# Performance work log

Hardware: AMD Instinct MI355X
Metric: run time of the kernel (lower is better)

## Reference

```python
import jax, jax.numpy as jnp
import numpy as np

PI = 3.141592653589793


def _conv2d(x, w, b=None, pad=0, groups=1):
    out = jax.lax.conv_general_dilated(
        x, w, (1, 1), ((pad, pad), (pad, pad)),
        dimension_numbers=('NCHW', 'OIHW', 'NCHW'), feature_group_count=groups)
    if b is not None:
        out = out + b[None, :, None, None]
    return out


def _l2norm(x, eps=1e-12):
    # torch F.normalize(p=2, dim=1)
    n = jnp.sqrt(jnp.sum(x * x, axis=1, keepdims=True))
    return x / jnp.maximum(n, eps)


def dense_sift(x):
    # Kornia DenseSIFTDescriptor defaults: 8 angular bins, 4x4 spatial bins,
    # spatial_bin_size=4, stride=1, padding=1, rootsift=True, clipval=0.2.
    eps = 1e-10
    nbins = 8
    # SpatialGradient('diff', normalized=False) with replicate padding:
    px = jnp.pad(x, ((0, 0), (0, 0), (0, 0), (1, 1)), mode='edge')
    gx = px[..., 2:] - px[..., :-2]
    py = jnp.pad(x, ((0, 0), (0, 0), (1, 1), (0, 0)), mode='edge')
    gy = py[:, :, 2:, :] - py[:, :, :-2, :]
    mag = jnp.sqrt(gx * gx + gy * gy + eps)
    ori = jnp.arctan2(gy, gx + eps) + 2.0 * PI
    o_big = nbins * ori / (2.0 * PI)
    bo0f = jnp.floor(o_big)
    wo1 = o_big - bo0f
    bo0 = jnp.mod(bo0f, nbins)
    bo1 = jnp.mod(bo0 + 1.0, nbins)
    w0 = (1.0 - wo1) * mag
    w1 = wo1 * mag
    bins = jnp.arange(nbins, dtype=x.dtype).reshape(1, nbins, 1, 1)
    # soft-assign gradient magnitude into 8 orientation bins  (B,8,H,W)
    ang = (bo0 == bins) * w0 + (bo1 == bins) * w1
    # AvgPool2d(4, stride=1, pad=2, count_include_pad=True) -> (B,8,H+1,W+1)
    avg_k = jnp.ones((nbins, 1, 4, 4), x.dtype) / 16.0
    pooled = _conv2d(ang, avg_k, pad=2, groups=nbins)
    # PoolingConv: identity-reshape 4x4 kernel, pad=1 -> 16 shifted copies of 8 chans
    B, _, Hp, Wp = pooled.shape
    H, W = Hp - 1, Wp - 1
    pp = jnp.pad(pooled, ((0, 0), (0, 0), (1, 1), (1, 1)))
    shifts = jnp.stack(
        [pp[:, :, i:i + H, j:j + W] for i in range(4) for j in range(4)], axis=2)
    out = shifts.reshape(B, nbins * 16, H, W)  # channel n = d*16 + i*4 + j
    out = jnp.clip(_l2norm(out), 0.0, 0.2)
    out = _l2norm(out)
    # rootsift: sqrt(L1-normalize + eps)
    l1 = jnp.sum(jnp.abs(out), axis=1, keepdims=True)
    return jnp.sqrt(out / jnp.maximum(l1, 1e-12) + eps)


def joint_bilateral_blur(x, guidance, ksize=5, sigma_color=0.1, sigma_space=1.5):
    # Kornia joint_bilateral_blur, border='reflect', color_distance='l1'
    r = ksize // 2
    ax = jnp.arange(ksize, dtype=x.dtype) - r
    g1 = jnp.exp(-(ax * ax) / (2.0 * sigma_space ** 2))
    g1 = g1 / jnp.sum(g1)
    space_k = jnp.outer(g1, g1)
    H, W = x.shape[-2], x.shape[-1]
    px = jnp.pad(x, ((0, 0), (0, 0), (r, r), (r, r)), mode='reflect')
    pg = jnp.pad(guidance, ((0, 0), (0, 0), (r, r), (r, r)), mode='reflect')
    num = jnp.zeros_like(x)
    den = jnp.zeros((x.shape[0], 1, H, W), x.dtype)
    inv = -0.5 / (sigma_color ** 2)
    for dy in range(ksize):
        for dx in range(ksize):
            gw = pg[:, :, dy:dy + H, dx:dx + W]
            cd = jnp.square(jnp.sum(jnp.abs(gw - guidance), axis=1, keepdims=True))
            k = space_k[dy, dx] * jnp.exp(inv * cd)
            num = num + px[:, :, dy:dy + H, dx:dx + W] * k
            den = den + k
    return num / den


def setup_inputs() -> dict:
    key = jax.random.key(0)
    ks = jax.random.split(key, 7)
    B, H, W = 4, 270, 512
    x = jax.random.uniform(ks[0], (B, 1, H, W), dtype=jnp.float32)
    def winit(k, shape):
        fan_in = shape[1] * shape[2] * shape[3]
        return jax.random.normal(k, shape, dtype=jnp.float32) / np.sqrt(fan_in)
    return {
        'x': x,
        'conv1_w': winit(ks[1], (32, 128, 5, 5)),
        'conv1_b': jax.random.normal(ks[2], (32,), dtype=jnp.float32) * 0.01,
        'conv2_w': winit(ks[3], (8, 32, 3, 3)),
        'conv2_b': jax.random.normal(ks[4], (8,), dtype=jnp.float32) * 0.01,
        'conv3_w': winit(ks[5], (2, 8, 5, 5)),
        'conv3_b': jax.random.normal(ks[6], (2,), dtype=jnp.float32) * 0.01,
    }


def reference(x, conv1_w, conv1_b, conv2_w, conv2_b, conv3_w, conv3_b):
    orig = x
    f = dense_sift(x)
    f = jax.nn.relu(_conv2d(f, conv1_w, conv1_b, pad=2))
    f = jax.nn.relu(_conv2d(f, conv2_w, conv2_b, pad=1))
    f = _conv2d(f, conv3_w, conv3_b, pad=2)
    f = joint_bilateral_blur(f, jnp.concatenate([orig, orig], axis=1))
    u = f[:, 0]
    u = jnp.clip((u - u.min()) / (u.max() - u.min() + 1e-6), 0.0, 1.0)
    u = u * (0.436 * 2.0) - 0.436
    v = f[:, 1]
    v = jnp.clip((v - v.min()) / (v.max() - v.min() + 1e-6), 0.0, 1.0)
    v = v * (0.615 * 2.0) - 0.615
    y = orig[:, 0]
    r = y + 1.14 * v
    g = y - 0.396 * u - 0.581 * v
    b = y + 2.029 * u
    return jnp.stack([r, g, b], axis=1)
```

## Files before the change

kernel.cpp:

```cpp
#include <hip/hip_runtime.h>
#include <hip/hip_bf16.h>

typedef __hip_bfloat16 bf16;
typedef __attribute__((ext_vector_type(8))) short short8v;
typedef __attribute__((ext_vector_type(4))) float f32x4;
typedef __attribute__((ext_vector_type(16))) float f32x16;

#define HH 270
#define WW 512
#define BB 4
#define HP 271
#define WP 513
#define NPIX (HH*WW)
#define NPOOL (HP*WP)
#define TWO_PI 6.28318530717958647692f
#define PLANE ((size_t)BB*NPIX*16)

__global__ void k_wprep(const float* __restrict__ w1, const float* __restrict__ w2,
                        const float* __restrict__ w3, short* __restrict__ apack,
                        short* __restrict__ a2pack, short* __restrict__ a3pack,
                        float* __restrict__ zp) {
    int stride = gridDim.x * blockDim.x;
    int t0 = blockIdx.x * blockDim.x + threadIdx.x;
    for (int i = t0; i < 1024; i += stride) zp[i] = 0.f;
    for (int i = t0; i < 8*25*64*8; i += stride) {
        int idx = i;
        int j    = idx & 7;  idx >>= 3;
        int lane = idx & 63; idx >>= 6;
        int t    = idx % 25;
        int ck   = idx / 25;
        int o = lane & 31;
        int c = ck*16 + (lane >> 5)*8 + j;
        float v = w1[o*3200 + c*25 + t];
        bf16 h = __float2bfloat16(v);
        apack[i] = *reinterpret_cast<short*>(&h);
    }
    for (int i = t0; i < 9*64*8; i += stride) {
        int j = i & 7; int l = (i >> 3) & 63; int tap = i >> 9;
        int o = l & 15; int cin = (l >> 4)*8 + j;
        float v = (o < 8) ? w2[o*288 + cin*9 + tap] : 0.f;
        bf16 h = __float2bfloat16(v);
        a2pack[i] = *reinterpret_cast<short*>(&h);
    }
    for (int i = t0; i < 7*64*8; i += stride) {
        int j = i & 7; int l = (i >> 3) & 63; int grp = i >> 9;
        int o = l & 15; int tap = grp*4 + (l >> 4);
        float v = (o < 2 && tap < 25) ? w3[o*200 + j*25 + tap] : 0.f;
        bf16 h = __float2bfloat16(v);
        a3pack[i] = *reinterpret_cast<short*>(&h);
    }
}

__global__ __launch_bounds__(256) void k_pool(const float* __restrict__ x,
                                              float* __restrict__ pooled) {
    __shared__ float hist[8][19][20];
    const int tx = threadIdx.x & 15, ty = threadIdx.x >> 4;
    const int j0 = blockIdx.x * 16, i0 = blockIdx.y * 16, b = blockIdx.z;
    const float* xb = x + (size_t)b * NPIX;

    for (int i = threadIdx.x; i < 8*19*20; i += 256) ((float*)hist)[i] = 0.f;
    __syncthreads();

    for (int i = threadIdx.x; i < 361; i += 256) {
        int lh = i / 19, lw = i - lh*19;
        int hh = i0 + lh - 2, ww = j0 + lw - 2;
        if (hh >= 0 && hh < HH && ww >= 0 && ww < WW) {
            float gx = xb[hh*WW + (ww+1 < WW ? ww+1 : WW-1)] - xb[hh*WW + (ww-1 >= 0 ? ww-1 : 0)];
            float gy = xb[(hh+1 < HH ? hh+1 : HH-1)*WW + ww] - xb[(hh-1 >= 0 ? hh-1 : 0)*WW + ww];
            float mag  = sqrtf(gx*gx + gy*gy + 1e-10f);
            float ori  = atan2f(gy, gx + 1e-10f) + TWO_PI;
            float obig = ori * (8.0f / TWO_PI);
            float b0f  = floorf(obig);
            float wo1  = obig - b0f;
            int ib0 = ((int)b0f) & 7;
            int ib1 = (ib0 + 1) & 7;
            hist[ib0][lh][lw] += (1.0f - wo1) * mag;
            hist[ib1][lh][lw] += wo1 * mag;
        }
    }
    __syncthreads();

    int i = i0 + ty, j = j0 + tx;
    if (i < HP && j < WP) {
        float a[8];
        #pragma unroll
        for (int c = 0; c < 8; ++c) a[c] = 0.f;
        #pragma unroll
        for (int di = 0; di < 4; ++di)
            #pragma unroll
            for (int dj = 0; dj < 4; ++dj) {
                #pragma unroll
                for (int c = 0; c < 8; ++c)
                    a[c] += hist[c][ty+di][tx+dj];
            }
        float* pb = pooled + (size_t)b*8*NPOOL + i*WP + j;
        const float s = 1.0f/16.0f;
        #pragma unroll
        for (int c = 0; c < 8; ++c) pb[c*NPOOL] = a[c]*s;
    }
}

__global__ __launch_bounds__(256) void k_feat(const float* __restrict__ pooled,
                                              short* __restrict__ f2) {
    __shared__ float T[8][19][19];
    const int tx = threadIdx.x & 15, ty = threadIdx.x >> 4;
    const int w0 = blockIdx.x * 16, h0 = blockIdx.y * 16, b = blockIdx.z;
    const float* pb = pooled + (size_t)b*8*NPOOL;

    for (int i = threadIdx.x; i < 8*361; i += 256) {
        int c = i / 361; int r = i - c*361; int lh = r / 19, lw = r - lh*19;
        int ph = h0 + lh - 1, pw = w0 + lw - 1;
        float v = 0.f;
        if (ph >= 0 && ph < HP && pw >= 0 && pw < WP)
            v = pb[c*NPOOL + ph*WP + pw];
        T[c][lh][lw] = v;
    }
    __syncthreads();

    float s2 = 0.f;
    #pragma unroll
    for (int c = 0; c < 8; ++c)
        #pragma unroll
        for (int i = 0; i < 4; ++i)
            #pragma unroll
            for (int j = 0; j < 4; ++j) {
                float u = T[c][ty+i][tx+j];
                s2 += u*u;
            }
    float inv1 = 1.0f / fmaxf(sqrtf(s2), 1e-12f);

    float sv2 = 0.f, sv1 = 0.f;
    #pragma unroll
    for (int c = 0; c < 8; ++c)
        #pragma unroll
        for (int i = 0; i < 4; ++i)
            #pragma unroll
            for (int j = 0; j < 4; ++j) {
                float u = T[c][ty+i][tx+j];
                float v = fminf(u*inv1, 0.2f);
                sv2 += v*v; sv1 += v;
            }
    float inv2  = 1.0f / fmaxf(sqrtf(sv2), 1e-12f);
    float invl1 = 1.0f / fmaxf(sv1 * inv2, 1e-12f);

    int outv[64];
    #pragma unroll
    for (int c = 0; c < 8; ++c)
        #pragma unroll
        for (int i = 0; i < 4; ++i)
            #pragma unroll
            for (int jj = 0; jj < 2; ++jj) {
                float u0 = T[c][ty+i][tx+jj*2];
                float u1 = T[c][ty+i][tx+jj*2+1];
                float v0 = fminf(u0*inv1, 0.2f) * inv2;
                float v1 = fminf(u1*inv1, 0.2f) * inv2;
                float fo0 = sqrtf(v0*invl1 + 1e-10f);
                float fo1 = sqrtf(v1*invl1 + 1e-10f);
                bf16 hb0 = __float2bfloat16(fo0);
                bf16 hb1 = __float2bfloat16(fo1);
                unsigned lo = *reinterpret_cast<unsigned short*>(&hb0);
                unsigned hi = *reinterpret_cast<unsigned short*>(&hb1);
                outv[c*8 + i*2 + jj] = (int)(lo | (hi << 16));
            }

    int h = h0 + ty, w = w0 + tx;
    if (h < HH) {
        const size_t pix = (size_t)b*NPIX + h*WW + w;
        #pragma unroll
        for (int ck = 0; ck < 8; ++ck) {
            int4* fb = reinterpret_cast<int4*>(f2 + (size_t)ck*PLANE + pix*16);
            int4 v0, v1;
            v0.x = outv[ck*8+0]; v0.y = outv[ck*8+1]; v0.z = outv[ck*8+2]; v0.w = outv[ck*8+3];
            v1.x = outv[ck*8+4]; v1.y = outv[ck*8+5]; v1.z = outv[ck*8+6]; v1.w = outv[ck*8+7];
            fb[0] = v0; fb[1] = v1;
        }
    }
}

__global__ __launch_bounds__(256, 2) void k_conv1(const short* __restrict__ f2,
        const short* __restrict__ apack, const float* __restrict__ bias,
        short* __restrict__ c1o, const short* __restrict__ zp16) {
    __shared__ short S[4][2][4608];
    const int tid = threadIdx.x;
    const int l   = tid & 63;
    const int wid = tid >> 6;
    const int n      = blockIdx.x;
    const int xcd    = n & 7;
    const int t_     = n >> 3;
    const int within = t_ & 7;
    const int g      = (t_ >> 3)*8 + xcd;
    const int b      = g / 34;
    const int ypair  = g - b*34;
    const int h0     = (ypair*2 + (within >> 2)) * 4;
    const int w0     = (within & 3) * 128;
    const int c32 = l & 31;
    const int ksel = l >> 5;
    const int gw0 = w0 + wid*32 - 2;

    short* Sw0 = &S[wid][0][0];
    short* Sw1 = &S[wid][1][0];

    f32x16 acc0 = {0.f};
    f32x16 acc1 = {0.f};
    f32x16 acc2 = {0.f};
    f32x16 acc3 = {0.f};

    auto STAGE = [&](int ck, short* dstbase) {
        const short* plane = f2 + (size_t)ck*PLANE;
        #pragma unroll
        for (int j = 0; j < 9; ++j) {
            int s  = j*64 + l;
            int pr = s / 72;
            int rem = s - pr*72;
            int px = rem >> 1;
            int half = rem & 1;
            int gh = h0 + pr - 2;
            int gw = gw0 + px;
            const short* src = ((unsigned)gh < (unsigned)HH && (unsigned)gw < (unsigned)WW)
                ? plane + (((size_t)b*HH + gh)*WW + gw)*16 + half*8
                : zp16;
            __builtin_amdgcn_global_load_lds(
                (const __attribute__((address_space(1))) void*)src,
                (__attribute__((address_space(3))) void*)(dstbase + j*512), 16, 0, 0);
        }
    };

    STAGE(0, Sw0);

    for (int ck = 0; ck < 8; ++ck) {
        short* cur = (ck & 1) ? Sw1 : Sw0;
        short* nxt = (ck & 1) ? Sw0 : Sw1;
        if (ck < 7) STAGE(ck + 1, nxt);
        asm volatile("s_waitcnt vmcnt(9)" ::: "memory");

        #pragma unroll
        for (int kx = 0; kx < 5; ++kx) {
            const int px = c32 + kx;
            const short* bp = cur + (size_t)px*16 + (size_t)ksel*8;
            short8v Bf[8];
            #pragma unroll
            for (int pr = 0; pr < 8; ++pr)
                Bf[pr] = *reinterpret_cast<const short8v*>(bp + pr*576);
            short8v Af[5];
            #pragma unroll
            for (int ky = 0; ky < 5; ++ky)
                Af[ky] = *reinterpret_cast<const short8v*>(
                    apack + ((size_t)(ck*25 + ky*5 + kx)*64 + l)*8);
            #pragma unroll
            for (int ky = 0; ky < 5; ++ky) {
                acc0 = __builtin_amdgcn_mfma_f32_32x32x16_bf16(Af[ky], Bf[ky+0], acc0, 0, 0, 0);
                acc1 = __builtin_amdgcn_mfma_f32_32x32x16_bf16(Af[ky], Bf[ky+1], acc1, 0, 0, 0);
                acc2 = __builtin_amdgcn_mfma_f32_32x32x16_bf16(Af[ky], Bf[ky+2], acc2, 0, 0, 0);
                acc3 = __builtin_amdgcn_mfma_f32_32x32x16_bf16(Af[ky], Bf[ky+3], acc3, 0, 0, 0);
            }
        }
        asm volatile("s_waitcnt lgkmcnt(0)" ::: "memory");
    }

    const int px = w0 + wid*32 + c32;
    #pragma unroll
    for (int r = 0; r < 4; ++r) {
        int h = h0 + r;
        if (h < HH) {
            const f32x16& A = (r==0) ? acc0 : (r==1) ? acc1 : (r==2) ? acc2 : acc3;
            const size_t rowbase = ((size_t)b*HH + h)*4;
            #pragma unroll
            for (int q = 0; q < 4; ++q) {
                short4 pk;
                short* pkp = (short*)&pk;
                #pragma unroll
                for (int j = 0; j < 4; ++j) {
                    float v = fmaxf(A[q*4 + j] + bias[q*8 + 4*ksel + j], 0.f);
                    bf16 hb = __float2bfloat16(v);
                    pkp[j] = *reinterpret_cast<short*>(&hb);
                }
                *reinterpret_cast<short4*>(c1o + ((rowbase + q)*WW + px)*8 + ksel*4) = pk;
            }
        }
    }
}

__global__ __launch_bounds__(256) void k_conv2m(const short* __restrict__ c1o,
        const short* __restrict__ a2pack, const float* __restrict__ bias,
        short* __restrict__ c2o, const short* __restrict__ zp16) {
    const int tid = threadIdx.x;
    const int l   = tid & 63;
    const int wid = tid >> 6;
    const int h   = blockIdx.y;
    const int b   = blockIdx.z;
    const int w0  = blockIdx.x*256 + wid*64;
    const int col = l & 15;
    const int kg  = l >> 4;

    f32x4 acc0 = {0.f,0.f,0.f,0.f};
    f32x4 acc1 = {0.f,0.f,0.f,0.f};
    f32x4 acc2 = {0.f,0.f,0.f,0.f};
    f32x4 acc3 = {0.f,0.f,0.f,0.f};

    #pragma unroll
    for (int ky = 0; ky < 3; ++ky) {
        int gh = h + ky - 1;
        bool rv = ((unsigned)gh < (unsigned)HH);
        const short* rowb = c1o + (((size_t)b*HH + (rv ? gh : 0))*4 + kg)*WW*8;
        #pragma unroll
        for (int kx = 0; kx < 3; ++kx) {
            short8v A = *reinterpret_cast<const short8v*>(
                a2pack + ((size_t)(ky*3 + kx)*64 + l)*8);
            #pragma unroll
            for (int nt = 0; nt < 4; ++nt) {
                int gw = w0 + nt*16 + col + kx - 1;
                const short* src = (rv && (unsigned)gw < (unsigned)WW)
                    ? rowb + (size_t)gw*8 : zp16;
                short8v B = *reinterpret_cast<const short8v*>(src);
                if (nt == 0) acc0 = __builtin_amdgcn_mfma_f32_16x16x32_bf16(A, B, acc0, 0, 0, 0);
                if (nt == 1) acc1 = __builtin_amdgcn_mfma_f32_16x16x32_bf16(A, B, acc1, 0, 0, 0);
                if (nt == 2) acc2 = __builtin_amdgcn_mfma_f32_16x16x32_bf16(A, B, acc2, 0, 0, 0);
                if (nt == 3) acc3 = __builtin_amdgcn_mfma_f32_16x16x32_bf16(A, B, acc3, 0, 0, 0);
            }
        }
    }

    if (kg < 2) {
        #pragma unroll
        for (int nt = 0; nt < 4; ++nt) {
            const f32x4& A = (nt==0) ? acc0 : (nt==1) ? acc1 : (nt==2) ? acc2 : acc3;
            int px = w0 + nt*16 + col;
            short4 pk;
            short* pkp = (short*)&pk;
            #pragma unroll
            for (int r = 0; r < 4; ++r) {
                float v = fmaxf(A[r] + bias[kg*4 + r], 0.f);
                bf16 hb = __float2bfloat16(v);
                pkp[r] = *reinterpret_cast<short*>(&hb);
            }
            *reinterpret_cast<short4*>(c2o + (((size_t)b*HH + h)*WW + px)*8 + kg*4) = pk;
        }
    }
}

__global__ __launch_bounds__(256) void k_conv3m(const short* __restrict__ c2o,
        const short* __restrict__ a3pack, const float* __restrict__ bias,
        float* __restrict__ c3o, const short* __restrict__ zp16) {
    const int tid = threadIdx.x;
    const int l   = tid & 63;
    const int wid = tid >> 6;
    const int h   = blockIdx.y;
    const int b   = blockIdx.z;
    const int w0  = blockIdx.x*256 + wid*64;
    const int col = l & 15;
    const int kg  = l >> 4;

    f32x4 acc0 = {0.f,0.f,0.f,0.f};
    f32x4 acc1 = {0.f,0.f,0.f,0.f};
    f32x4 acc2 = {0.f,0.f,0.f,0.f};
    f32x4 acc3 = {0.f,0.f,0.f,0.f};

    #pragma unroll
    for (int grp = 0; grp < 7; ++grp) {
        int tap = grp*4 + kg;
        int ky = tap / 5, kx = tap - ky*5;
        int gh = h + ky - 2;
        bool tv = (tap < 25) && ((unsigned)gh < (unsigned)HH);
        const short* rowb = c2o + ((size_t)b*HH + (tv ? gh : 0))*WW*8;
        short8v A = *reinterpret_cast<const short8v*>(
            a3pack + ((size_t)grp*64 + l)*8);
        #pragma unroll
        for (int nt = 0; nt < 4; ++nt) {
            int gw = w0 + nt*16 + col + kx - 2;
            const short* src = (tv && (unsigned)gw < (unsigned)WW)
                ? rowb + (size_t)gw*8 : zp16;
            short8v B = *reinterpret_cast<const short8v*>(src);
            if (nt == 0) acc0 = __builtin_amdgcn_mfma_f32_16x16x32_bf16(A, B, acc0, 0, 0, 0);
            if (nt == 1) acc1 = __builtin_amdgcn_mfma_f32_16x16x32_bf16(A, B, acc1, 0, 0, 0);
            if (nt == 2) acc2 = __builtin_amdgcn_mfma_f32_16x16x32_bf16(A, B, acc2, 0, 0, 0);
            if (nt == 3) acc3 = __builtin_amdgcn_mfma_f32_16x16x32_bf16(A, B, acc3, 0, 0, 0);
        }
    }

    if (kg == 0) {
        #pragma unroll
        for (int nt = 0; nt < 4; ++nt) {
            const f32x4& A = (nt==0) ? acc0 : (nt==1) ? acc1 : (nt==2) ? acc2 : acc3;
            int px = w0 + nt*16 + col;
            c3o[((size_t)b*2 + 0)*NPIX + h*WW + px] = A[0] + bias[0];
            c3o[((size_t)b*2 + 1)*NPIX + h*WW + px] = A[1] + bias[1];
        }
    }
}

__device__ __forceinline__ int refl(int i, int n) {
    if (i < 0) i = -i;
    if (i >= n) i = 2*n - 2 - i;
    return i;
}

__global__ void k_bilat(const float* __restrict__ c3, const float* __restrict__ x,
                        float* __restrict__ outb) {
    int idx = blockIdx.x * blockDim.x + threadIdx.x;
    if (idx >= BB*NPIX) return;
    int b = idx / NPIX;
    int p = idx - b*NPIX;
    int h = p / WW, w = p - h*WW;
    const float* xb = x + (size_t)b*NPIX;
    const float* f0 = c3 + (size_t)b*2*NPIX;
    const float* f1 = f0 + NPIX;

    float e1 = expf(-1.0f/4.5f), e2 = expf(-4.0f/4.5f);
    float sden = 1.0f + 2.f*e1 + 2.f*e2;
    float g1v[5] = { e2/sden, e1/sden, 1.0f/sden, e1/sden, e2/sden };

    float g = xb[p];
    float num0 = 0.f, num1 = 0.f, den = 0.f;
    #pragma unroll
    for (int dy = 0; dy < 5; ++dy) {
        int hh = refl(h + dy - 2, HH);
        #pragma unroll
        for (int dx = 0; dx < 5; ++dx) {
            int wc = refl(w + dx - 2, WW);
            float gs = xb[hh*WW + wc];
            float d = gs - g;
            float k = g1v[dy] * g1v[dx] * expf(-200.0f * d * d);
            num0 += f0[hh*WW + wc] * k;
            num1 += f1[hh*WW + wc] * k;
            den  += k;
        }
    }
    float invd = 1.0f / den;
    outb[(size_t)b*2*NPIX + p]        = num0 * invd;
    outb[(size_t)b*2*NPIX + NPIX + p] = num1 * invd;
}

__global__ void k_minmax1(const float* __restrict__ blur, float4* __restrict__ partial) {
    float umin = 3.0e38f, umax = -3.0e38f, vmin = 3.0e38f, vmax = -3.0e38f;
    for (int i = blockIdx.x*blockDim.x + threadIdx.x; i < BB*NPIX; i += gridDim.x*blockDim.x) {
        int b = i / NPIX; int p = i - b*NPIX;
        float u = blur[(size_t)b*2*NPIX + p];
        float v = blur[(size_t)b*2*NPIX + NPIX + p];
        umin = fminf(umin, u); umax = fmaxf(umax, u);
        vmin = fminf(vmin, v); vmax = fmaxf(vmax, v);
    }
    #pragma unroll
    for (int off = 32; off > 0; off >>= 1) {
        umin = fminf(umin, __shfl_down(umin, off));
        umax = fmaxf(umax, __shfl_down(umax, off));
        vmin = fminf(vmin, __shfl_down(vmin, off));
        vmax = fmaxf(vmax, __shfl_down(vmax, off));
    }
    __shared__ float4 sm[4];
    int lane = threadIdx.x & 63, wid = threadIdx.x >> 6;
    if (lane == 0) sm[wid] = make_float4(umin, umax, vmin, vmax);
    __syncthreads();
    if (threadIdx.x == 0) {
        float4 r = sm[0];
        for (int k = 1; k < 4; ++k) {
            r.x = fminf(r.x, sm[k].x); r.y = fmaxf(r.y, sm[k].y);
            r.z = fminf(r.z, sm[k].z); r.w = fmaxf(r.w, sm[k].w);
        }
        partial[blockIdx.x] = r;
    }
}

__global__ void k_minmax2(const float4* __restrict__ partial, float* __restrict__ sc) {
    float4 p = partial[threadIdx.x];
    #pragma unroll
    for (int off = 32; off > 0; off >>= 1) {
        p.x = fminf(p.x, __shfl_down(p.x, off));
        p.y = fmaxf(p.y, __shfl_down(p.y, off));
        p.z = fminf(p.z, __shfl_down(p.z, off));
        p.w = fmaxf(p.w, __shfl_down(p.w, off));
    }
    __shared__ float4 sm[2];
    if ((threadIdx.x & 63) == 0) sm[threadIdx.x >> 6] = p;
    __syncthreads();
    if (threadIdx.x == 0) {
        sc[0] = fminf(sm[0].x, sm[1].x);
        sc[1] = fmaxf(sm[0].y, sm[1].y);
        sc[2] = fminf(sm[0].z, sm[1].z);
        sc[3] = fmaxf(sm[0].w, sm[1].w);
    }
}

__global__ void k_final(const float* __restrict__ blur, const float* __restrict__ x,
                        const float* __restrict__ sc, float* __restrict__ out) {
    int idx = blockIdx.x * blockDim.x + threadIdx.x;
    if (idx >= BB*NPIX) return;
    int b = idx / NPIX;
    int p = idx - b*NPIX;
    float umin = sc[0], umax = sc[1], vmin = sc[2], vmax = sc[3];
    float u = blur[(size_t)b*2*NPIX + p];
    float v = blur[(size_t)b*2*NPIX + NPIX + p];
    u = fminf(fmaxf((u - umin) / (umax - umin + 1e-6f), 0.f), 1.f) * 0.872f - 0.436f;
    v = fminf(fmaxf((v - vmin) / (vmax - vmin + 1e-6f), 0.f), 1.f) * 1.23f  - 0.615f;
    float y = x[(size_t)b*NPIX + p];
    out[(size_t)(b*3+0)*NPIX + p] = y + 1.14f*v;
    out[(size_t)(b*3+1)*NPIX + p] = y - 0.396f*u - 0.581f*v;
    out[(size_t)(b*3+2)*NPIX + p] = y + 2.029f*u;
}

extern "C" void kernel_launch(void* const* d_in, const int* in_sizes, int n_in,
                              void* d_out, int out_size, void* d_ws, size_t ws_size,
                              hipStream_t stream) {
    const float* x  = (const float*)d_in[0];
    const float* w1 = (const float*)d_in[1];
    const float* b1 = (const float*)d_in[2];
    const float* w2 = (const float*)d_in[3];
    const float* b2 = (const float*)d_in[4];
    const float* w3 = (const float*)d_in[5];
    const float* b3 = (const float*)d_in[6];
    float* out = (float*)d_out;
    char* ws = (char*)d_ws;

    const size_t POOLED_OFF = 0;
    const size_t X_OFF      = 17795072;
    const size_t Y_OFF      = X_OFF + 141557760;
    const size_t AP_OFF     = Y_OFF + 35389440;
    const size_t A2_OFF     = AP_OFF + 204800;
    const size_t A3_OFF     = A2_OFF + 9216;
    const size_t PART_OFF   = A3_OFF + 7168;
    const size_t SC_OFF     = PART_OFF + 2048;
    const size_t ZP_OFF     = SC_OFF + 256;

    float*  pooled = (float*)(ws + POOLED_OFF);
    short*  f2     = (short*)(ws + X_OFF);
    short*  c2o    = (short*)(ws + X_OFF);
    float*  c3o    = (float*)(ws + X_OFF + 24000000);
    float*  blur   = (float*)(ws + X_OFF + 32000000);
    short*  c1o    = (short*)(ws + Y_OFF);
    short*  apack  = (short*)(ws + AP_OFF);
    short*  a2p    = (short*)(ws + A2_OFF);
    short*  a3p    = (short*)(ws + A3_OFF);
    float4* part   = (float4*)(ws + PART_OFF);
    float*  sc     = (float*)(ws + SC_OFF);
    float*  zp     = (float*)(ws + ZP_OFF);

    k_wprep<<<512, 256, 0, stream>>>(w1, w2, w3, apack, a2p, a3p, zp);

    dim3 pg((WP + 15)/16, (HP + 15)/16, BB);
    k_pool<<<pg, 256, 0, stream>>>(x, pooled);

    dim3 fg(WW/16, (HH + 15)/16, BB);
    k_feat<<<fg, 256, 0, stream>>>(pooled, f2);

    k_conv1<<<1088, 256, 0, stream>>>(f2, apack, b1, c1o, (const short*)zp);

    dim3 c2g(WW/256, HH, BB);
    k_conv2m<<<c2g, 256, 0, stream>>>(c1o, a2p, b2, c2o, (const short*)zp);
    k_conv3m<<<c2g, 256, 0, stream>>>(c2o, a3p, b3, c3o, (const short*)zp);

    k_bilat<<<(BB*NPIX + 255)/256, 256, 0, stream>>>(c3o, x, blur);
    k_minmax1<<<128, 256, 0, stream>>>(blur, part);
    k_minmax2<<<1, 128, 0, stream>>>(part, sc);
    k_final<<<(BB*NPIX + 255)/256, 256, 0, stream>>>(blur, x, sc, out);
}
```

Measured before the change: 289.0 us.

## Enlarge conv1 per-wave tile to 4x64 and drop LDS double buffering

Each conv1 wave now computes a 4-row by 64-pixel tile with two N-subtiles sharing the same A fragments, so weight loads are reused across twice as many outputs. The block covers 8 rows by 128 columns and the grid shrinks to 576 blocks, with some blocks exiting early. The per-wave LDS buffer grows to a single 136-pixel-wide staging area, and the double-buffered prefetch is replaced by a synchronous stage-then-wait for each channel chunk. The starting chunk is staggered per wave to spread weight and L2 traffic. The trade is more A-fragment reuse and fewer blocks, at the cost of losing load/compute overlap and of higher register pressure from eight accumulators.

```diff
diff --git a/kernel.cpp b/kernel.cpp
--- a/kernel.cpp
+++ b/kernel.cpp
@@ -180,7 +180,7 @@
 __global__ __launch_bounds__(256, 2) void k_conv1(const short* __restrict__ f2,
         const short* __restrict__ apack, const float* __restrict__ bias,
         short* __restrict__ c1o, const short* __restrict__ zp16) {
-    __shared__ short S[4][2][4608];
+    __shared__ short S[4][8704];
     const int tid = threadIdx.x;
     const int l   = tid & 63;
     const int wid = tid >> 6;
@@ -189,29 +189,29 @@
     const int t_     = n >> 3;
     const int within = t_ & 7;
     const int g      = (t_ >> 3)*8 + xcd;
-    const int b      = g / 34;
-    const int ypair  = g - b*34;
-    const int h0     = (ypair*2 + (within >> 2)) * 4;
+    if (g >= 68) return;
+    const int b      = g / 17;
+    const int yq     = g - b*17;
+    const int h0b    = (yq*2 + (within >> 2)) * 8;
     const int w0     = (within & 3) * 128;
     const int c32 = l & 31;
     const int ksel = l >> 5;
-    const int gw0 = w0 + wid*32 - 2;
-
-    short* Sw0 = &S[wid][0][0];
-    short* Sw1 = &S[wid][1][0];
-
-    f32x16 acc0 = {0.f};
-    f32x16 acc1 = {0.f};
-    f32x16 acc2 = {0.f};
-    f32x16 acc3 = {0.f};
-
-    auto STAGE = [&](int ck, short* dstbase) {
+    const int rh  = wid >> 1;
+    const int ph  = wid & 1;
+    const int h0  = h0b + rh*4;
+    const int gw0 = w0 + ph*64 - 2;
+    short* Sw = &S[wid][0];
+
+    f32x16 a00 = {0.f}, a10 = {0.f}, a20 = {0.f}, a30 = {0.f};
+    f32x16 a01 = {0.f}, a11 = {0.f}, a21 = {0.f}, a31 = {0.f};
+
+    auto STAGE = [&](int ck) {
         const short* plane = f2 + (size_t)ck*PLANE;
         #pragma unroll
-        for (int j = 0; j < 9; ++j) {
+        for (int j = 0; j < 17; ++j) {
             int s  = j*64 + l;
-            int pr = s / 72;
-            int rem = s - pr*72;
+            int pr = s / 136;
+            int rem = s - pr*136;
             int px = rem >> 1;
             int half = rem & 1;
             int gh = h0 + pr - 2;
@@ -221,60 +221,77 @@
                 : zp16;
             __builtin_amdgcn_global_load_lds(
                 (const __attribute__((address_space(1))) void*)src,
-                (__attribute__((address_space(3))) void*)(dstbase + j*512), 16, 0, 0);
+                (__attribute__((address_space(3))) void*)(Sw + j*512), 16, 0, 0);
         }
     };
 
-    STAGE(0, Sw0);
-
-    for (int ck = 0; ck < 8; ++ck) {
-        short* cur = (ck & 1) ? Sw1 : Sw0;
-        short* nxt = (ck & 1) ? Sw0 : Sw1;
-        if (ck < 7) STAGE(ck + 1, nxt);
-        asm volatile("s_waitcnt vmcnt(9)" ::: "memory");
+    for (int ci = 0; ci < 8; ++ci) {
+        const int ck = (ci + wid*2) & 7;
+        STAGE(ck);
+        asm volatile("s_waitcnt vmcnt(0)" ::: "memory");
 
         #pragma unroll
         for (int kx = 0; kx < 5; ++kx) {
-            const int px = c32 + kx;
-            const short* bp = cur + (size_t)px*16 + (size_t)ksel*8;
-            short8v Bf[8];
-            #pragma unroll
-            for (int pr = 0; pr < 8; ++pr)
-                Bf[pr] = *reinterpret_cast<const short8v*>(bp + pr*576);
             short8v Af[5];
             #pragma unroll
             for (int ky = 0; ky < 5; ++ky)
                 Af[ky] = *reinterpret_cast<const short8v*>(
                     apack + ((size_t)(ck*25 + ky*5 + kx)*64 + l)*8);
-            #pragma unroll
-            for (int ky = 0; ky < 5; ++ky) {
-                acc0 = __builtin_amdgcn_mfma_f32_32x32x16_bf16(Af[ky], Bf[ky+0], acc0, 0, 0, 0);
-                acc1 = __builtin_amdgcn_mfma_f32_32x32x16_bf16(Af[ky], Bf[ky+1], acc1, 0, 0, 0);
-                acc2 = __builtin_amdgcn_mfma_f32_32x32x16_bf16(Af[ky], Bf[ky+2], acc2, 0, 0, 0);
-                acc3 = __builtin_amdgcn_mfma_f32_32x32x16_bf16(Af[ky], Bf[ky+3], acc3, 0, 0, 0);
+            {
+                const short* bp = Sw + (size_t)(c32 + kx)*16 + (size_t)ksel*8;
+                short8v Bf[8];
+                #pragma unroll
+                for (int pr = 0; pr < 8; ++pr)
+                    Bf[pr] = *reinterpret_cast<const short8v*>(bp + pr*1088);
+                #pragma unroll
+                for (int ky = 0; ky < 5; ++ky) {
+                    a00 = __builtin_amdgcn_mfma_f32_32x32x16_bf16(Af[ky], Bf[ky+0], a00, 0, 0, 0);
+                    a10 = __builtin_amdgcn_mfma_f32_32x32x16_bf16(Af[ky], Bf[ky+1], a10, 0, 0, 0);
+                    a20 = __builtin_amdgcn_mfma_f32_32x32x16_bf16(Af[ky], Bf[ky+2], a20, 0, 0, 0);
+                    a30 = __builtin_amdgcn_mfma_f32_32x32x16_bf16(Af[ky], Bf[ky+3], a30, 0, 0, 0);
+                }
+            }
+            {
+                const short* bp = Sw + (size_t)(32 + c32 + kx)*16 + (size_t)ksel*8;
+                short8v Bf[8];
+                #pragma unroll
+                for (int pr = 0; pr < 8; ++pr)
+                    Bf[pr] = *reinterpret_cast<const short8v*>(bp + pr*1088);
+                #pragma unroll
+                for (int ky = 0; ky < 5; ++ky) {
+                    a01 = __builtin_amdgcn_mfma_f32_32x32x16_bf16(Af[ky], Bf[ky+0], a01, 0, 0, 0);
+                    a11 = __builtin_amdgcn_mfma_f32_32x32x16_bf16(Af[ky], Bf[ky+1], a11, 0, 0, 0);
+                    a21 = __builtin_amdgcn_mfma_f32_32x32x16_bf16(Af[ky], Bf[ky+2], a21, 0, 0, 0);
+                    a31 = __builtin_amdgcn_mfma_f32_32x32x16_bf16(Af[ky], Bf[ky+3], a31, 0, 0, 0);
+                }
             }
         }
         asm volatile("s_waitcnt lgkmcnt(0)" ::: "memory");
     }
 
-    const int px = w0 + wid*32 + c32;
     #pragma unroll
     for (int r = 0; r < 4; ++r) {
         int h = h0 + r;
         if (h < HH) {
-            const f32x16& A = (r==0) ? acc0 : (r==1) ? acc1 : (r==2) ? acc2 : acc3;
             const size_t rowbase = ((size_t)b*HH + h)*4;
             #pragma unroll
-            for (int q = 0; q < 4; ++q) {
-                short4 pk;
-                short* pkp = (short*)&pk;
+            for (int nt = 0; nt < 2; ++nt) {
+                const f32x16& A = (nt==0)
+                    ? ((r==0) ? a00 : (r==1) ? a10 : (r==2) ? a20 : a30)
+                    : ((r==0) ? a01 : (r==1) ? a11 : (r==2) ? a21 : a31);
+                int px = w0 + ph*64 + nt*32 + c32;
                 #pragma unroll
-                for (int j = 0; j < 4; ++j) {
-                    float v = fmaxf(A[q*4 + j] + bias[q*8 + 4*ksel + j], 0.f);
-                    bf16 hb = __float2bfloat16(v);
-                    pkp[j] = *reinterpret_cast<short*>(&hb);
+                for (int q = 0; q < 4; ++q) {
+                    short4 pk;
+                    short* pkp = (short*)&pk;
+                    #pragma unroll
+                    for (int j = 0; j < 4; ++j) {
+                        float v = fmaxf(A[q*4 + j] + bias[q*8 + 4*ksel + j], 0.f);
+                        bf16 hb = __float2bfloat16(v);
+                        pkp[j] = *reinterpret_cast<short*>(&hb);
+                    }
+                    *reinterpret_cast<short4*>(c1o + ((rowbase + q)*WW + px)*8 + ksel*4) = pk;
                 }
-                *reinterpret_cast<short4*>(c1o + ((rowbase + q)*WW + px)*8 + ksel*4) = pk;
             }
         }
     }
@@ -541,7 +558,7 @@
     dim3 fg(WW/16, (HH + 15)/16, BB);
     k_feat<<<fg, 256, 0, stream>>>(pooled, f2);
 
-    k_conv1<<<1088, 256, 0, stream>>>(f2, apack, b1, c1o, (const short*)zp);
+    k_conv1<<<576, 256, 0, stream>>>(f2, apack, b1, c1o, (const short*)zp);
 
     dim3 c2g(WW/256, HH, BB);
     k_conv2m<<<c2g, 256, 0, stream>>>(c1o, a2p, b2, c2o, (const short*)zp);
```

Measured after the change: 320.3 us. 1.11x slower.
